# Performance work log

Measured on AMD Instinct MI355X. Metric: run time of the kernel, lower is better.

Reference implementation:

```python
import jax, jax.numpy as jnp
import numpy as np

E_PHI = 1024
E_F = 1024
HID = 1024
N_HEADS = 16
HEAD_DIM = HID // N_HEADS


def setup_inputs() -> dict:
    key = jax.random.key(0)
    ks = jax.random.split(key, 9)
    B, S = 2, 2048
    s = 0.02
    return {
        "q": jax.random.normal(ks[0], (B, S, E_PHI), jnp.float32),
        "k": jax.random.normal(ks[1], (B, S, E_PHI), jnp.float32),
        "v": jax.random.normal(ks[2], (B, S, E_F), jnp.float32),
        "W_q": jax.random.normal(ks[3], (E_PHI, HID), jnp.float32) * s,
        "W_k": jax.random.normal(ks[4], (E_PHI, HID), jnp.float32) * s,
        "W_v": jax.random.normal(ks[5], (E_F, HID), jnp.float32) * s,
        "b_v": jax.random.normal(ks[6], (HID,), jnp.float32) * s,
        "W_o": jax.random.normal(ks[7], (HID, E_F), jnp.float32) * s,
        "b_o": jax.random.normal(ks[8], (E_F,), jnp.float32) * s,
    }


def reference(q, k, v, W_q, W_k, W_v, b_v, W_o, b_o):
    B, S, _ = q.shape
    # projections -> [B, S, n_heads, head_dim]
    qh = (q @ W_q).reshape(B, S, N_HEADS, HEAD_DIM)
    kh = (k @ W_k).reshape(B, S, N_HEADS, HEAD_DIM)
    vh = (v @ W_v + b_v).reshape(B, S, N_HEADS, HEAD_DIM)

    scale = 1.0 / jnp.sqrt(jnp.float32(HEAD_DIM))
    # scores: [B, H, S_q, S_k]
    scores = jnp.einsum("bihd,bjhd->bhij", qh, kh) * scale

    i = jnp.arange(S)[:, None]
    j = jnp.arange(S)[None, :]
    # strict causal (j < i) plus the single (0,0) entry
    keep = (j < i) | ((i == 0) & (j == 0))
    scores = jnp.where(keep, scores, jnp.float32(-jnp.inf))

    probs = jax.nn.softmax(scores, axis=-1)
    attn = jnp.einsum("bhij,bjhd->bihd", probs, vh).reshape(B, S, HID)
    # dropout is identity in eval mode
    return attn @ W_o + b_o
```

## Files before the change

### kernel.cpp

```cpp
#include <hip/hip_runtime.h>
#include <hip/hip_bf16.h>

typedef __attribute__((ext_vector_type(8))) short bf16x8;
typedef __attribute__((ext_vector_type(4))) float f32x4;
typedef __attribute__((ext_vector_type(4))) unsigned u32x4;

typedef __attribute__((address_space(1))) const void gv_t;
typedef __attribute__((address_space(3))) void lv_t;

static __device__ __forceinline__ void gload16(const void* g, void* l) {
    __builtin_amdgcn_global_load_lds((gv_t*)g, (lv_t*)l, 16, 0, 0);
}

static __device__ __forceinline__ f32x4 mfma16(bf16x8 a, bf16x8 b, f32x4 c) {
    return __builtin_amdgcn_mfma_f32_16x16x32_bf16(a, b, c, 0, 0, 0);
}

static __device__ __forceinline__ unsigned short f2bf(float x) {
    __bf16 b = (__bf16)x;
    return __builtin_bit_cast(unsigned short, b);
}
static __device__ __forceinline__ unsigned pk2(float lo, float hi) {
    return (unsigned)f2bf(lo) | ((unsigned)f2bf(hi) << 16);
}

#define NN 1024
#define KK 1024
#define BK 32
#define NKT (KK / BK)
#define AP 72
#define SOFF2 17.3123404907f

__global__ void prep_k(const float* __restrict__ q, const float* __restrict__ k,
                       const float* __restrict__ v, unsigned short* __restrict__ qkvb,
                       const float* __restrict__ w0, const float* __restrict__ w1,
                       const float* __restrict__ w2, const float* __restrict__ w3,
                       unsigned short* __restrict__ Wt)
{
    __shared__ float t[32][33];
    const int id = blockIdx.x;
    if (id < 6144) {
        const int z = id >> 11;
        const int xb = id & 2047;
        const float* src = (z == 0) ? q : (z == 1) ? k : v;
        unsigned short* d = qkvb + (size_t)z * 4194304u;
        const size_t i = ((size_t)xb * 256 + threadIdx.x) * 8;
        float4 a = *reinterpret_cast<const float4*>(&src[i]);
        float4 b = *reinterpret_cast<const float4*>(&src[i + 4]);
        bf16x8 o;
        o[0] = (short)f2bf(a.x); o[1] = (short)f2bf(a.y);
        o[2] = (short)f2bf(a.z); o[3] = (short)f2bf(a.w);
        o[4] = (short)f2bf(b.x); o[5] = (short)f2bf(b.y);
        o[6] = (short)f2bf(b.z); o[7] = (short)f2bf(b.w);
        *reinterpret_cast<bf16x8*>(&d[i]) = o;
    } else {
        const int tt2 = id - 6144;
        const int z  = tt2 >> 10;
        const int bx = tt2 & 31, by = (tt2 >> 5) & 31;
        const float* W = (z == 0) ? w0 : (z == 1) ? w1 : (z == 2) ? w2 : w3;
        unsigned short* D = Wt + (size_t)z * 1048576u;
        const int tx = threadIdx.x & 31, ty = threadIdx.x >> 5;
        const int x  = bx * 32 + tx;
        const int y0 = by * 32;
        for (int i = ty; i < 32; i += 8) t[i][tx] = W[(size_t)(y0 + i) * 1024 + x];
        __syncthreads();
        const int xo = y0 + tx;
        for (int i = ty; i < 32; i += 8)
            D[(size_t)(bx * 32 + i) * 1024 + xo] = f2bf(t[tx][i]);
    }
}

__global__ __launch_bounds__(256, 3)
void gemm_proj_k(const unsigned short* __restrict__ Abase,
                 const unsigned short* __restrict__ Btbase,
                 unsigned short* __restrict__ Cbase,
                 unsigned short* __restrict__ C2,
                 const float* __restrict__ bias)
{
    __shared__ unsigned short As[3][4096];
    __shared__ unsigned short Bs[3][4096];

    const int f   = blockIdx.x;
    const int xcd = f & 7;
    const int g   = f >> 3;
    const int z   = g >> 5;
    const int rr  = g & 31;
    const int bx  = xcd * 4 + (rr & 3);
    const int by  = rr >> 2;

    const unsigned short* A  = Abase  + (size_t)z * 4194304u;
    const unsigned short* Bt = Btbase + (size_t)z * 1048576u;

    const int tid = threadIdx.x;
    const int wid = tid >> 6, lane = tid & 63;
    const int lg = lane >> 4, lc = lane & 15;
    const int brow = bx * 128;
    const int bcol = by * 128;
    const int wr = (wid >> 1) * 64;
    const int wc = (wid & 1) * 64;

    const int srow = tid >> 2;
    const int scol = (tid & 3) * 8;

    f32x4 acc[4][4];
#pragma unroll
    for (int i = 0; i < 4; ++i)
#pragma unroll
        for (int j = 0; j < 4; ++j) acc[i][j] = (f32x4){0.f, 0.f, 0.f, 0.f};

    auto issue_tile = [&](int kt, int c) {
        const int k0 = kt * BK;
        gload16(&A [(size_t)(brow + srow)      * KK + k0 + scol], &As[c][tid * 8]);
        gload16(&A [(size_t)(brow + 64 + srow) * KK + k0 + scol], &As[c][2048 + tid * 8]);
        gload16(&Bt[(size_t)(bcol + srow)      * KK + k0 + scol], &Bs[c][tid * 8]);
        gload16(&Bt[(size_t)(bcol + 64 + srow) * KK + k0 + scol], &Bs[c][2048 + tid * 8]);
    };
    auto compute_tile = [&](int c) {
        bf16x8 af[4], bfr[4];
#pragma unroll
        for (int i = 0; i < 4; ++i)
            af[i] = *reinterpret_cast<const bf16x8*>(&As[c][(wr + i * 16 + lc) * 32 + lg * 8]);
#pragma unroll
        for (int j = 0; j < 4; ++j)
            bfr[j] = *reinterpret_cast<const bf16x8*>(&Bs[c][(wc + j * 16 + lc) * 32 + lg * 8]);
#pragma unroll
        for (int i = 0; i < 4; ++i)
#pragma unroll
            for (int j = 0; j < 4; ++j)
                acc[i][j] = mfma16(af[i], bfr[j], acc[i][j]);
    };

    issue_tile(0, 0);
    issue_tile(1, 1);

    int c0 = 0, c1 = 1, c2 = 2;
    for (int kt = 0; kt < NKT - 1; ++kt) {
        asm volatile("s_waitcnt vmcnt(4)" ::: "memory");
        __builtin_amdgcn_s_barrier();
        __builtin_amdgcn_sched_barrier(0);
        if (kt + 2 < NKT) issue_tile(kt + 2, c2);
        compute_tile(c0);
        const int t = c0; c0 = c1; c1 = c2; c2 = t;
    }
    asm volatile("s_waitcnt vmcnt(0)" ::: "memory");
    __builtin_amdgcn_s_barrier();
    __builtin_amdgcn_sched_barrier(0);
    compute_tile(c0);

    const float scale = (z == 0) ? 0.18033688f : 1.0f;

    if (z == 2) {
#pragma unroll
        for (int j = 0; j < 4; ++j) {
            const int col = bcol + wc + j * 16 + lc;
            const int h = col >> 6, d = col & 63;
            const float bb = bias[col];
#pragma unroll
            for (int i = 0; i < 4; ++i) {
                const int row0 = brow + wr + i * 16 + lg * 4;
                const int b = row0 >> 11, s0 = row0 & 2047;
                const size_t o = ((size_t)((b * 16 + h) * 64 + d)) * 2048u + s0;
                uint2 st;
                st.x = pk2(acc[i][j][0] + bb, acc[i][j][1] + bb);
                st.y = pk2(acc[i][j][2] + bb, acc[i][j][3] + bb);
                *reinterpret_cast<uint2*>(&C2[o]) = st;
            }
        }
    } else {
#pragma unroll
        for (int j = 0; j < 4; ++j) {
            const int col = bcol + wc + j * 16 + lc;
#pragma unroll
            for (int i = 0; i < 4; ++i) {
                const int row0 = brow + wr + i * 16 + lg * 4;
#pragma unroll
                for (int r = 0; r < 4; ++r)
                    Cbase[(size_t)z * 4194304u + (size_t)(row0 + r) * NN + col] =
                        f2bf(acc[i][j][r] * scale);
            }
        }
    }
}

__global__ __launch_bounds__(256, 2)
void gemm_out_k(const unsigned short* __restrict__ A,
                const unsigned short* __restrict__ Bt,
                float* __restrict__ C,
                const float* __restrict__ bias)
{
    __shared__ unsigned short As[3][2048];
    __shared__ unsigned short Bs[3][4096];

    const int f = blockIdx.x, xcd = f & 7, g = f >> 3;
    const int bx = xcd * 8 + (g & 7);
    const int by = g >> 3;
    const int tid = threadIdx.x;
    const int wid = tid >> 6, lane = tid & 63;
    const int lg = lane >> 4, lc = lane & 15;
    const int brow = bx * 64, bcol = by * 128;
    const int wc = wid * 32;

    const int srow = tid >> 2;
    const int scol = (tid & 3) * 8;

    f32x4 acc[4][2];
#pragma unroll
    for (int i = 0; i < 4; ++i)
#pragma unroll
        for (int j = 0; j < 2; ++j) acc[i][j] = (f32x4){0.f, 0.f, 0.f, 0.f};

    auto issue_tile = [&](int kt, int c) {
        const int k0 = kt * BK;
        gload16(&A [(size_t)(brow + srow)      * KK + k0 + scol], &As[c][tid * 8]);
        gload16(&Bt[(size_t)(bcol + srow)      * KK + k0 + scol], &Bs[c][tid * 8]);
        gload16(&Bt[(size_t)(bcol + 64 + srow) * KK + k0 + scol], &Bs[c][2048 + tid * 8]);
    };
    auto compute_tile = [&](int c) {
        bf16x8 af[4], bfr[2];
#pragma unroll
        for (int i = 0; i < 4; ++i)
            af[i] = *reinterpret_cast<const bf16x8*>(&As[c][(i * 16 + lc) * 32 + lg * 8]);
#pragma unroll
        for (int j = 0; j < 2; ++j)
            bfr[j] = *reinterpret_cast<const bf16x8*>(&Bs[c][(wc + j * 16 + lc) * 32 + lg * 8]);
#pragma unroll
        for (int i = 0; i < 4; ++i)
#pragma unroll
            for (int j = 0; j < 2; ++j)
                acc[i][j] = mfma16(af[i], bfr[j], acc[i][j]);
    };

    issue_tile(0, 0);
    issue_tile(1, 1);

    int c0 = 0, c1 = 1, c2 = 2;
    for (int kt = 0; kt < NKT - 1; ++kt) {
        asm volatile("s_waitcnt vmcnt(3)" ::: "memory");
        __builtin_amdgcn_s_barrier();
        __builtin_amdgcn_sched_barrier(0);
        if (kt + 2 < NKT) issue_tile(kt + 2, c2);
        compute_tile(c0);
        const int t = c0; c0 = c1; c1 = c2; c2 = t;
    }
    asm volatile("s_waitcnt vmcnt(0)" ::: "memory");
    __builtin_amdgcn_s_barrier();
    __builtin_amdgcn_sched_barrier(0);
    compute_tile(c0);

#pragma unroll
    for (int j = 0; j < 2; ++j) {
        const int col = bcol + wc + j * 16 + lc;
        const float bb = bias[col];
#pragma unroll
        for (int i = 0; i < 4; ++i) {
            const int row0 = brow + i * 16 + lg * 4;
#pragma unroll
            for (int r = 0; r < 4; ++r)
                C[(size_t)(row0 + r) * NN + col] = acc[i][j][r] + bb;
        }
    }
}

__global__ __launch_bounds__(256, 4)
void attn_k(const unsigned short* __restrict__ qh,
            const unsigned short* __restrict__ kh,
            const unsigned short* __restrict__ vt,
            unsigned short* __restrict__ out)
{
    __shared__ unsigned short Ks[2][64 * AP];
    __shared__ unsigned short Vs[2][64 * AP];

    const int id = blockIdx.x;
    const int u  = id >> 5;
    const int qt = (u < 16) ? u : 47 - u;
    const int bh = (id & 7) * 4 + ((id >> 3) & 3);
    const int b = bh >> 4, h = bh & 15;
    const int tid = threadIdx.x, wid = tid >> 6, lane = tid & 63;
    const int lg = lane >> 4, lc = lane & 15;
    const int q0w = qt * 64 + wid * 16;

    const size_t base = (size_t)b * 2048u * 1024u + (size_t)h * 64u;
    const unsigned short* Qb  = qh + base;
    const unsigned short* Kb  = kh + base;
    const unsigned short* Vtb = vt + (size_t)bh * 131072u;

    const int r0 = tid >> 3, kof = (tid & 7) * 8;
    const int kperm = ((r0 & 12) << 1) | ((r0 >> 2) & 4) | (r0 & 3);

    bf16x8 qf[2];
#pragma unroll
    for (int s = 0; s < 2; ++s)
        qf[s] = *reinterpret_cast<const bf16x8*>(&Qb[(size_t)(q0w + lc) * 1024 + s * 32 + lg * 8]);

    f32x4 accT[4];
#pragma unroll
    for (int d = 0; d < 4; ++d) accT[d] = (f32x4){0.f, 0.f, 0.f, 0.f};
    float lsum = 0.f;

    bf16x8 ka0 = *reinterpret_cast<const bf16x8*>(&Kb [(size_t)(kperm)      * 1024 + kof]);
    bf16x8 ka1 = *reinterpret_cast<const bf16x8*>(&Kb [(size_t)(32 + kperm) * 1024 + kof]);
    bf16x8 va0 = *reinterpret_cast<const bf16x8*>(&Vtb[(size_t)(r0)      * 2048 + kof]);
    bf16x8 va1 = *reinterpret_cast<const bf16x8*>(&Vtb[(size_t)(32 + r0) * 2048 + kof]);

    for (int kt = 0; kt <= qt; ++kt) {
        const int cur = kt & 1;
        const int k0 = kt * 64;

        *reinterpret_cast<bf16x8*>(&Ks[cur][(r0)      * AP + kof]) = ka0;
        *reinterpret_cast<bf16x8*>(&Ks[cur][(32 + r0) * AP + kof]) = ka1;
        *reinterpret_cast<bf16x8*>(&Vs[cur][(r0)      * AP + kof]) = va0;
        *reinterpret_cast<bf16x8*>(&Vs[cur][(32 + r0) * AP + kof]) = va1;
        asm volatile("s_waitcnt lgkmcnt(0)" ::: "memory");
        __builtin_amdgcn_s_barrier();
        __builtin_amdgcn_sched_barrier(0);

        if (kt < qt) {
            const int kn = k0 + 64;
            ka0 = *reinterpret_cast<const bf16x8*>(&Kb [(size_t)(kn + kperm)      * 1024 + kof]);
            ka1 = *reinterpret_cast<const bf16x8*>(&Kb [(size_t)(kn + 32 + kperm) * 1024 + kof]);
            va0 = *reinterpret_cast<const bf16x8*>(&Vtb[(size_t)(r0)      * 2048 + kn + kof]);
            va1 = *reinterpret_cast<const bf16x8*>(&Vtb[(size_t)(32 + r0) * 2048 + kn + kof]);
        }

        f32x4 sc[4];
#pragma unroll
        for (int g = 0; g < 4; ++g) sc[g] = (f32x4){0.f, 0.f, 0.f, 0.f};
        __builtin_amdgcn_s_setprio(1);
#pragma unroll
        for (int s = 0; s < 2; ++s)
#pragma unroll
            for (int g = 0; g < 4; ++g) {
                bf16x8 kf = *reinterpret_cast<const bf16x8*>(
                    &Ks[cur][(g * 16 + lc) * AP + s * 32 + lg * 8]);
                sc[g] = mfma16(kf, qf[s], sc[g]);
            }
        __builtin_amdgcn_s_setprio(0);

        if (kt == qt) {
            const int qi = q0w + lc;
#pragma unroll
            for (int g = 0; g < 4; ++g)
#pragma unroll
                for (int r = 0; r < 4; ++r) {
                    const int ki = k0 + ((g & 2) << 4) + 8 * lg + 4 * (g & 1) + r;
                    const bool keep = (ki < qi) || (qi == 0 && ki == 0);
                    if (!keep) sc[g][r] = -1e30f;
                }
        }

        float p[4][4];
#pragma unroll
        for (int g = 0; g < 4; ++g)
#pragma unroll
            for (int r = 0; r < 4; ++r) {
                p[g][r] = exp2f(sc[g][r] - SOFF2);
                lsum += p[g][r];
            }

#pragma unroll
        for (int s = 0; s < 2; ++s) {
            u32x4 fr;
            fr[0] = pk2(p[2 * s][0],     p[2 * s][1]);
            fr[1] = pk2(p[2 * s][2],     p[2 * s][3]);
            fr[2] = pk2(p[2 * s + 1][0], p[2 * s + 1][1]);
            fr[3] = pk2(p[2 * s + 1][2], p[2 * s + 1][3]);
            bf16x8 pb = __builtin_bit_cast(bf16x8, fr);
            __builtin_amdgcn_s_setprio(1);
#pragma unroll
            for (int di = 0; di < 4; ++di) {
                bf16x8 vf = *reinterpret_cast<const bf16x8*>(
                    &Vs[cur][(di * 16 + lc) * AP + s * 32 + lg * 8]);
                accT[di] = mfma16(vf, pb, accT[di]);
            }
            __builtin_amdgcn_s_setprio(0);
        }
    }

    lsum += __shfl_xor(lsum, 16);
    lsum += __shfl_xor(lsum, 32);
    const float inv = 1.0f / lsum;

    const size_t orow = (size_t)(b * 2048 + q0w + lc) * 1024 + (size_t)h * 64 + lg * 4;
#pragma unroll
    for (int di = 0; di < 4; ++di) {
        unsigned lo  = pk2(accT[di][0] * inv, accT[di][1] * inv);
        unsigned hi2 = pk2(accT[di][2] * inv, accT[di][3] * inv);
        uint2 st; st.x = lo; st.y = hi2;
        *reinterpret_cast<uint2*>(&out[orow + di * 16]) = st;
    }
}

extern "C" void kernel_launch(void* const* d_in, const int* in_sizes, int n_in,
                              void* d_out, int out_size, void* d_ws, size_t ws_size,
                              hipStream_t stream)
{
    const float* q   = (const float*)d_in[0];
    const float* k   = (const float*)d_in[1];
    const float* v   = (const float*)d_in[2];
    const float* W_q = (const float*)d_in[3];
    const float* W_k = (const float*)d_in[4];
    const float* W_v = (const float*)d_in[5];
    const float* b_v = (const float*)d_in[6];
    const float* W_o = (const float*)d_in[7];
    const float* b_o = (const float*)d_in[8];

    char* w = (char*)d_ws;
    unsigned short* qkvb = (unsigned short*)w;
    unsigned short* Wt   = (unsigned short*)(w + 25165824);
    unsigned short* ph   = (unsigned short*)(w + 33554432);
    unsigned short* attn = (unsigned short*)(w + 58720256);
    unsigned short* vt   = ph + 2 * 4194304;

    prep_k <<<dim3(10240, 1, 1), 256, 0, stream>>>(q, k, v, qkvb, W_q, W_k, W_v, W_o, Wt);
    gemm_proj_k<<<dim3(768, 1, 1), 256, 0, stream>>>(qkvb, Wt, ph, vt, b_v);
    attn_k <<<dim3(1024, 1, 1), 256, 0, stream>>>(ph, ph + 4194304, vt, attn);
    gemm_out_k<<<dim3(512, 1, 1), 256, 0, stream>>>(attn, Wt + 3 * 1048576, (float*)d_out, b_o);
}
```

Baseline: 110.3 us.

## Split attention key tiles across waves with per-wave LDS and cross-wave reduction

The attention kernel now gives each wave every fourth key tile for all 64 query rows of the block, instead of giving each wave 16 query rows over all key tiles. K and V tiles go straight from global memory into per-wave XOR-swizzled LDS with direct global-to-LDS loads, and block-wide barriers are gone from the main loop. Partial outputs and row sums are combined through LDS at the end. This costs more registers (launch bounds drop to 2 blocks per SIMD), a final reduction pass, and lower occupancy.

```diff
diff --git a/kernel.cpp b/kernel.cpp
--- a/kernel.cpp
+++ b/kernel.cpp
@@ -28,7 +28,6 @@
 #define KK 1024
 #define BK 32
 #define NKT (KK / BK)
-#define AP 72
 #define SOFF2 17.3123404907f
 
 __global__ void prep_k(const float* __restrict__ q, const float* __restrict__ k,
@@ -261,14 +260,13 @@
     }
 }
 
-__global__ __launch_bounds__(256, 4)
+__global__ __launch_bounds__(256, 2)
 void attn_k(const unsigned short* __restrict__ qh,
             const unsigned short* __restrict__ kh,
             const unsigned short* __restrict__ vt,
             unsigned short* __restrict__ out)
 {
-    __shared__ unsigned short Ks[2][64 * AP];
-    __shared__ unsigned short Vs[2][64 * AP];
+    __shared__ unsigned short S[4][8192];
 
     const int id = blockIdx.x;
     const int u  = id >> 5;
@@ -277,114 +275,167 @@
     const int b = bh >> 4, h = bh & 15;
     const int tid = threadIdx.x, wid = tid >> 6, lane = tid & 63;
     const int lg = lane >> 4, lc = lane & 15;
-    const int q0w = qt * 64 + wid * 16;
+    const int q0 = qt * 64;
 
     const size_t base = (size_t)b * 2048u * 1024u + (size_t)h * 64u;
     const unsigned short* Qb  = qh + base;
     const unsigned short* Kb  = kh + base;
     const unsigned short* Vtb = vt + (size_t)bh * 131072u;
 
-    const int r0 = tid >> 3, kof = (tid & 7) * 8;
-    const int kperm = ((r0 & 12) << 1) | ((r0 >> 2) & 4) | (r0 & 3);
-
-    bf16x8 qf[2];
-#pragma unroll
-    for (int s = 0; s < 2; ++s)
-        qf[s] = *reinterpret_cast<const bf16x8*>(&Qb[(size_t)(q0w + lc) * 1024 + s * 32 + lg * 8]);
-
-    f32x4 accT[4];
-#pragma unroll
-    for (int d = 0; d < 4; ++d) accT[d] = (f32x4){0.f, 0.f, 0.f, 0.f};
-    float lsum = 0.f;
-
-    bf16x8 ka0 = *reinterpret_cast<const bf16x8*>(&Kb [(size_t)(kperm)      * 1024 + kof]);
-    bf16x8 ka1 = *reinterpret_cast<const bf16x8*>(&Kb [(size_t)(32 + kperm) * 1024 + kof]);
-    bf16x8 va0 = *reinterpret_cast<const bf16x8*>(&Vtb[(size_t)(r0)      * 2048 + kof]);
-    bf16x8 va1 = *reinterpret_cast<const bf16x8*>(&Vtb[(size_t)(32 + r0) * 2048 + kof]);
-
-    for (int kt = 0; kt <= qt; ++kt) {
-        const int cur = kt & 1;
+    unsigned short* Ks = &S[wid][0];
+    unsigned short* Vs = &S[wid][4096];
+
+    const int Lr  = lane >> 3;
+    const int swz = ((lane & 7) ^ Lr) * 8;
+    int koff[8], voff[8];
+#pragma unroll
+    for (int i = 0; i < 8; ++i) {
+        const int p = 8 * i + Lr;
+        const int key = (p & 32) | ((p & 12) << 1) | ((p >> 2) & 4) | (p & 3);
+        koff[i] = key * 1024 + swz;
+        voff[i] = p * 2048 + swz;
+    }
+
+    auto issue_loads = [&](int kt) {
         const int k0 = kt * 64;
-
-        *reinterpret_cast<bf16x8*>(&Ks[cur][(r0)      * AP + kof]) = ka0;
-        *reinterpret_cast<bf16x8*>(&Ks[cur][(32 + r0) * AP + kof]) = ka1;
-        *reinterpret_cast<bf16x8*>(&Vs[cur][(r0)      * AP + kof]) = va0;
-        *reinterpret_cast<bf16x8*>(&Vs[cur][(32 + r0) * AP + kof]) = va1;
+#pragma unroll
+        for (int i = 0; i < 8; ++i)
+            gload16(&Kb[(size_t)k0 * 1024 + koff[i]], &Ks[i * 512]);
+#pragma unroll
+        for (int i = 0; i < 8; ++i)
+            gload16(&Vtb[(size_t)voff[i] + k0], &Vs[i * 512]);
+    };
+
+    bf16x8 qf[4][2];
+#pragma unroll
+    for (int f = 0; f < 4; ++f)
+#pragma unroll
+        for (int s = 0; s < 2; ++s)
+            qf[f][s] = *reinterpret_cast<const bf16x8*>(
+                &Qb[(size_t)(q0 + f * 16 + lc) * 1024 + s * 32 + lg * 8]);
+
+    f32x4 accT[4][4];
+#pragma unroll
+    for (int f = 0; f < 4; ++f)
+#pragma unroll
+        for (int d = 0; d < 4; ++d) accT[f][d] = (f32x4){0.f, 0.f, 0.f, 0.f};
+    float lsum[4] = {0.f, 0.f, 0.f, 0.f};
+
+    int kt = wid;
+    if (kt <= qt) issue_loads(kt);
+    for (; kt <= qt; kt += 4) {
+        asm volatile("s_waitcnt vmcnt(0)" ::: "memory");
+        __builtin_amdgcn_sched_barrier(0);
+
+        bf16x8 kf[4][2], vf[4][2];
+#pragma unroll
+        for (int g = 0; g < 4; ++g)
+#pragma unroll
+            for (int s = 0; s < 2; ++s) {
+                const int off = (g * 16 + lc) * 64 + (((s * 4 + lg) ^ (lc & 7)) * 8);
+                kf[g][s] = *reinterpret_cast<const bf16x8*>(&Ks[off]);
+                vf[g][s] = *reinterpret_cast<const bf16x8*>(&Vs[off]);
+            }
         asm volatile("s_waitcnt lgkmcnt(0)" ::: "memory");
-        __builtin_amdgcn_s_barrier();
         __builtin_amdgcn_sched_barrier(0);
-
-        if (kt < qt) {
-            const int kn = k0 + 64;
-            ka0 = *reinterpret_cast<const bf16x8*>(&Kb [(size_t)(kn + kperm)      * 1024 + kof]);
-            ka1 = *reinterpret_cast<const bf16x8*>(&Kb [(size_t)(kn + 32 + kperm) * 1024 + kof]);
-            va0 = *reinterpret_cast<const bf16x8*>(&Vtb[(size_t)(r0)      * 2048 + kn + kof]);
-            va1 = *reinterpret_cast<const bf16x8*>(&Vtb[(size_t)(32 + r0) * 2048 + kn + kof]);
+        if (kt + 4 <= qt) issue_loads(kt + 4);
+
+        const int k0 = kt * 64;
+        const bool diag = (kt == qt);
+
+#pragma unroll
+        for (int f = 0; f < 4; ++f) {
+            f32x4 sc[4];
+#pragma unroll
+            for (int g = 0; g < 4; ++g) sc[g] = (f32x4){0.f, 0.f, 0.f, 0.f};
+            __builtin_amdgcn_s_setprio(1);
+#pragma unroll
+            for (int s = 0; s < 2; ++s)
+#pragma unroll
+                for (int g = 0; g < 4; ++g)
+                    sc[g] = mfma16(kf[g][s], qf[f][s], sc[g]);
+            __builtin_amdgcn_s_setprio(0);
+
+            if (diag) {
+                const int qi = q0 + f * 16 + lc;
+#pragma unroll
+                for (int g = 0; g < 4; ++g)
+#pragma unroll
+                    for (int r = 0; r < 4; ++r) {
+                        const int ki = k0 + ((g & 2) << 4) + 8 * lg + 4 * (g & 1) + r;
+                        const bool keep = (ki < qi) || (qi == 0 && ki == 0);
+                        if (!keep) sc[g][r] = -1e30f;
+                    }
+            }
+
+            float p[4][4];
+#pragma unroll
+            for (int g = 0; g < 4; ++g)
+#pragma unroll
+                for (int r = 0; r < 4; ++r) {
+                    p[g][r] = exp2f(sc[g][r] - SOFF2);
+                    lsum[f] += p[g][r];
+                }
+
+#pragma unroll
+            for (int s = 0; s < 2; ++s) {
+                u32x4 fr;
+                fr[0] = pk2(p[2 * s][0],     p[2 * s][1]);
+                fr[1] = pk2(p[2 * s][2],     p[2 * s][3]);
+                fr[2] = pk2(p[2 * s + 1][0], p[2 * s + 1][1]);
+                fr[3] = pk2(p[2 * s + 1][2], p[2 * s + 1][3]);
+                bf16x8 pb = __builtin_bit_cast(bf16x8, fr);
+                __builtin_amdgcn_s_setprio(1);
+#pragma unroll
+                for (int di = 0; di < 4; ++di)
+                    accT[f][di] = mfma16(vf[di][s], pb, accT[f][di]);
+                __builtin_amdgcn_s_setprio(0);
+            }
         }
-
-        f32x4 sc[4];
-#pragma unroll
-        for (int g = 0; g < 4; ++g) sc[g] = (f32x4){0.f, 0.f, 0.f, 0.f};
-        __builtin_amdgcn_s_setprio(1);
-#pragma unroll
-        for (int s = 0; s < 2; ++s)
-#pragma unroll
-            for (int g = 0; g < 4; ++g) {
-                bf16x8 kf = *reinterpret_cast<const bf16x8*>(
-                    &Ks[cur][(g * 16 + lc) * AP + s * 32 + lg * 8]);
-                sc[g] = mfma16(kf, qf[s], sc[g]);
-            }
-        __builtin_amdgcn_s_setprio(0);
-
-        if (kt == qt) {
-            const int qi = q0w + lc;
-#pragma unroll
-            for (int g = 0; g < 4; ++g)
-#pragma unroll
-                for (int r = 0; r < 4; ++r) {
-                    const int ki = k0 + ((g & 2) << 4) + 8 * lg + 4 * (g & 1) + r;
-                    const bool keep = (ki < qi) || (qi == 0 && ki == 0);
-                    if (!keep) sc[g][r] = -1e30f;
-                }
+    }
+
+#pragma unroll
+    for (int f = 0; f < 4; ++f) {
+        float ls = lsum[f];
+        ls += __shfl_xor(ls, 16);
+        ls += __shfl_xor(ls, 32);
+        lsum[f] = ls;
+    }
+    float* R = (float*)&S[wid][0];
+#pragma unroll
+    for (int f = 0; f < 4; ++f) {
+        if (f == wid) continue;
+        const int slot = (f < wid) ? f : f - 1;
+#pragma unroll
+        for (int di = 0; di < 4; ++di)
+            *reinterpret_cast<f32x4*>(&R[slot * 1024 + lc * 64 + di * 16 + lg * 4]) = accT[f][di];
+        R[3072 + slot * 16 + lc] = lsum[f];
+    }
+    __syncthreads();
+
+    float ltot = lsum[wid];
+    f32x4 osum[4];
+#pragma unroll
+    for (int di = 0; di < 4; ++di) osum[di] = accT[wid][di];
+#pragma unroll
+    for (int s = 0; s < 4; ++s) {
+        if (s == wid) continue;
+        const float* Rs = (const float*)&S[s][0];
+        const int slot = (wid < s) ? wid : wid - 1;
+#pragma unroll
+        for (int di = 0; di < 4; ++di) {
+            f32x4 v = *reinterpret_cast<const f32x4*>(&Rs[slot * 1024 + lc * 64 + di * 16 + lg * 4]);
+            osum[di] += v;
         }
-
-        float p[4][4];
-#pragma unroll
-        for (int g = 0; g < 4; ++g)
-#pragma unroll
-            for (int r = 0; r < 4; ++r) {
-                p[g][r] = exp2f(sc[g][r] - SOFF2);
-                lsum += p[g][r];
-            }
-
-#pragma unroll
-        for (int s = 0; s < 2; ++s) {
-            u32x4 fr;
-            fr[0] = pk2(p[2 * s][0],     p[2 * s][1]);
-            fr[1] = pk2(p[2 * s][2],     p[2 * s][3]);
-            fr[2] = pk2(p[2 * s + 1][0], p[2 * s + 1][1]);
-            fr[3] = pk2(p[2 * s + 1][2], p[2 * s + 1][3]);
-            bf16x8 pb = __builtin_bit_cast(bf16x8, fr);
-            __builtin_amdgcn_s_setprio(1);
-#pragma unroll
-            for (int di = 0; di < 4; ++di) {
-                bf16x8 vf = *reinterpret_cast<const bf16x8*>(
-                    &Vs[cur][(di * 16 + lc) * AP + s * 32 + lg * 8]);
-                accT[di] = mfma16(vf, pb, accT[di]);
-            }
-            __builtin_amdgcn_s_setprio(0);
-        }
-    }
-
-    lsum += __shfl_xor(lsum, 16);
-    lsum += __shfl_xor(lsum, 32);
-    const float inv = 1.0f / lsum;
-
-    const size_t orow = (size_t)(b * 2048 + q0w + lc) * 1024 + (size_t)h * 64 + lg * 4;
+        ltot += Rs[3072 + slot * 16 + lc];
+    }
+
+    const float inv = 1.0f / ltot;
+    const size_t orow = (size_t)(b * 2048 + q0 + wid * 16 + lc) * 1024 + (size_t)h * 64 + lg * 4;
 #pragma unroll
     for (int di = 0; di < 4; ++di) {
-        unsigned lo  = pk2(accT[di][0] * inv, accT[di][1] * inv);
-        unsigned hi2 = pk2(accT[di][2] * inv, accT[di][3] * inv);
+        unsigned lo  = pk2(osum[di][0] * inv, osum[di][1] * inv);
+        unsigned hi2 = pk2(osum[di][2] * inv, osum[di][3] * inv);
         uint2 st; st.x = lo; st.y = hi2;
         *reinterpret_cast<uint2*>(&out[orow + di * 16]) = st;
     }
```

After: 151.9 us. +37.6%, slower.
